# Kernel optimization log

Measured on AMD Instinct MI355X. Metric: run time of the kernel, lower is better.

## Reference

```python
import jax, jax.numpy as jnp
import numpy as np

M, K, N = 4096, 4096, 11008  # tokens, in_features, out_features


def setup_inputs() -> dict:
    key = jax.random.key(0)
    k0, k1, k2 = jax.random.split(key, 3)
    # quint8 activations: values in [0, 255], zero_point 128
    x_q = jax.random.randint(k0, (M, K), 0, 256, dtype=jnp.int32)
    # qint8 weight: values in [-128, 127], zero_point 0 (as prepacked in __init__)
    w_q = jax.random.randint(k1, (N, K), -128, 128, dtype=jnp.int32)
    bias = jax.random.normal(k2, (N,), dtype=jnp.float32) * 0.1
    return {
        "x_q": x_q,
        "w_q": w_q,
        "bias": bias,
        "x_scale": jnp.float32(0.02),
        "w_scale": jnp.float32(0.01),
        "out_scale": jnp.float32(1.0),   # self.scale = 1.0
        "x_zero_point": 128,
        "out_zero_point": 0,             # self.zero_point = 0
    }


def reference(x_q, w_q, bias, x_scale, w_scale, out_scale, x_zero_point, out_zero_point):
    # int8 GEMM with int32 accumulation: (x - zp_x) @ W^T
    acc = jnp.einsum(
        "mk,nk->mn",
        x_q - x_zero_point,
        w_q,
        preferred_element_type=jnp.int32,
    )
    # dequantize + bias (fp32), then requantize to quint8 output
    y = acc.astype(jnp.float32) * (x_scale * w_scale) + bias
    q = jnp.clip(jnp.round(y / out_scale) + out_zero_point, 0, 255).astype(jnp.int32)
    return q
```

## Files before the change

kernel.cpp:

```cpp
#include <hip/hip_runtime.h>

#define M_DIM 4096
#define K_DIM 4096
#define N_DIM 11008
#define BM 256
#define BN 128
#define BK 64
#define NTILES (K_DIM / BK)

typedef int v4i  __attribute__((ext_vector_type(4)));
typedef int v16i __attribute__((ext_vector_type(16)));

#define WAIT_VM6 0x3F76
#define WAIT_VM0 0x3F70

__device__ __forceinline__ void load_lds16(const void* g, void* l) {
    __builtin_amdgcn_global_load_lds(
        (const __attribute__((address_space(1))) void*)g,
        (__attribute__((address_space(3))) void*)l,
        16, 0, 0);
}

__device__ __forceinline__ unsigned int pack4(int4 v, int zp) {
    return ((unsigned int)(v.x - zp) & 0xFF)
         | (((unsigned int)(v.y - zp) & 0xFF) << 8)
         | (((unsigned int)(v.z - zp) & 0xFF) << 16)
         | (((unsigned int)(v.w - zp) & 0xFF) << 24);
}

__global__ void pack_both_kernel(const int* __restrict__ x, const int* __restrict__ w,
                                 unsigned int* __restrict__ x8, unsigned int* __restrict__ w8,
                                 const int* __restrict__ zp_p, int nx16, int nw16) {
    int i = blockIdx.x * blockDim.x + threadIdx.x;
    if (i < nx16) {
        const int zp = zp_p[0];
        const int4* p = (const int4*)x + i * 4;
        uint4 o;
        o.x = pack4(p[0], zp);
        o.y = pack4(p[1], zp);
        o.z = pack4(p[2], zp);
        o.w = pack4(p[3], zp);
        ((uint4*)x8)[i] = o;
    } else {
        int j = i - nx16;
        if (j >= nw16) return;
        const int4* p = (const int4*)w + j * 4;
        uint4 o;
        o.x = pack4(p[0], 0);
        o.y = pack4(p[1], 0);
        o.z = pack4(p[2], 0);
        o.w = pack4(p[3], 0);
        ((uint4*)w8)[j] = o;
    }
}

__global__ __launch_bounds__(256, 2) void gemm_i8_kernel(
    const signed char* __restrict__ A8,
    const signed char* __restrict__ B8,
    const float* __restrict__ bias,
    const float* __restrict__ xs_p, const float* __restrict__ ws_p,
    const float* __restrict__ os_p, const int* __restrict__ ozp_p,
    int* __restrict__ out) {
    __shared__ v4i As0[BM * BK / 16];
    __shared__ v4i Bs0[BN * BK / 16];
    __shared__ v4i As1[BM * BK / 16];
    __shared__ v4i Bs1[BN * BK / 16];

    const int tid  = threadIdx.x;
    const int lane = tid & 63;
    const int wave = tid >> 6;

    const int bid   = blockIdx.x;
    const int xcd   = bid & 7;
    const int local = bid >> 3;
    const int m_blk = xcd * 2 + (local >= 86 ? 1 : 0);
    const int n_blk = (local >= 86) ? (local - 86) : local;
    const int m0 = m_blk * BM;
    const int n0 = n_blk * BN;

    long offA[4], offB[2];
    int  ldsA[4], ldsB[2];
#pragma unroll
    for (int j = 0; j < 4; ++j) {
        const int s   = tid + 256 * j;
        const int row = s >> 2;
        const int gg  = (s & 3) ^ ((row >> 1) & 3);
        offA[j] = (long)(m0 + row) * K_DIM + gg * 16;
        ldsA[j] = s;
    }
#pragma unroll
    for (int j = 0; j < 2; ++j) {
        const int s   = tid + 256 * j;
        const int row = s >> 2;
        const int gg  = (s & 3) ^ ((row >> 1) & 3);
        offB[j] = (long)(n0 + row) * K_DIM + gg * 16;
        ldsB[j] = s;
    }

    const int waveM = wave >> 1, waveN = wave & 1;
    const int l31 = lane & 31, h = lane >> 5;
    int aSlot[4][2], bSlot[2][2];
#pragma unroll
    for (int mt = 0; mt < 4; ++mt) {
        const int rA = waveM * 128 + mt * 32 + l31;
#pragma unroll
        for (int s = 0; s < 2; ++s) {
            const int g = 2 * s + h;
            aSlot[mt][s] = rA * 4 + (g ^ ((rA >> 1) & 3));
        }
    }
#pragma unroll
    for (int nt = 0; nt < 2; ++nt) {
        const int rB = waveN * 64 + nt * 32 + l31;
#pragma unroll
        for (int s = 0; s < 2; ++s) {
            const int g = 2 * s + h;
            bSlot[nt][s] = rB * 4 + (g ^ ((rB >> 1) & 3));
        }
    }

    v16i acc[4][2];
#pragma unroll
    for (int mt = 0; mt < 4; ++mt)
#pragma unroll
        for (int nt = 0; nt < 2; ++nt)
#pragma unroll
            for (int r = 0; r < 16; ++r) acc[mt][nt][r] = 0;

    auto stage = [&](int tile, v4i* Asb, v4i* Bsb) {
        const long koff = (long)tile * BK;
#pragma unroll
        for (int j = 0; j < 4; ++j) load_lds16(A8 + offA[j] + koff, (char*)(Asb + ldsA[j]));
#pragma unroll
        for (int j = 0; j < 2; ++j) load_lds16(B8 + offB[j] + koff, (char*)(Bsb + ldsB[j]));
    };
    auto compute = [&](const v4i* Asb, const v4i* Bsb) {
#pragma unroll
        for (int s = 0; s < 2; ++s) {
            v4i a[4], b[2];
#pragma unroll
            for (int mt = 0; mt < 4; ++mt) a[mt] = Asb[aSlot[mt][s]];
#pragma unroll
            for (int nt = 0; nt < 2; ++nt) b[nt] = Bsb[bSlot[nt][s]];
#pragma unroll
            for (int mt = 0; mt < 4; ++mt)
#pragma unroll
                for (int nt = 0; nt < 2; ++nt)
                    acc[mt][nt] = __builtin_amdgcn_mfma_i32_32x32x32_i8(
                        a[mt], b[nt], acc[mt][nt], 0, 0, 0);
        }
    };

    stage(0, As0, Bs0);
    stage(1, As1, Bs1);

#pragma unroll 1
    for (int kk = 0; kk < 31; ++kk) {
        const int k = 2 * kk;
        __builtin_amdgcn_s_waitcnt(WAIT_VM6);
        __builtin_amdgcn_s_barrier();
        compute(As0, Bs0);
        __builtin_amdgcn_s_barrier();
        stage(k + 2, As0, Bs0);
        __builtin_amdgcn_s_waitcnt(WAIT_VM6);
        __builtin_amdgcn_s_barrier();
        compute(As1, Bs1);
        __builtin_amdgcn_s_barrier();
        stage(k + 3, As1, Bs1);
    }
    __builtin_amdgcn_s_waitcnt(WAIT_VM6);
    __builtin_amdgcn_s_barrier();
    compute(As0, Bs0);
    __builtin_amdgcn_s_waitcnt(WAIT_VM0);
    __builtin_amdgcn_s_barrier();
    compute(As1, Bs1);

    const float scale  = xs_p[0] * ws_p[0];
    const float inv_os = 1.0f / os_p[0];
    const int   ozp    = ozp_p[0];
#pragma unroll
    for (int mt = 0; mt < 4; ++mt) {
        const int rbase = m0 + waveM * 128 + mt * 32 + 4 * h;
#pragma unroll
        for (int nt = 0; nt < 2; ++nt) {
            const int col = n0 + waveN * 64 + nt * 32 + l31;
            const float bv = bias[col];
#pragma unroll
            for (int r = 0; r < 16; ++r) {
                const int row = rbase + (r & 3) + 8 * (r >> 2);
                float y = (float)acc[mt][nt][r] * scale + bv;
                int q = (int)rintf(y * inv_os) + ozp;
                q = q < 0 ? 0 : (q > 255 ? 255 : q);
                out[(long)row * N_DIM + col] = q;
            }
        }
    }
}

extern "C" void kernel_launch(void* const* d_in, const int* in_sizes, int n_in,
                              void* d_out, int out_size, void* d_ws, size_t ws_size,
                              hipStream_t stream) {
    const int*   x_q  = (const int*)d_in[0];
    const int*   w_q  = (const int*)d_in[1];
    const float* bias = (const float*)d_in[2];
    const float* xs   = (const float*)d_in[3];
    const float* wsc  = (const float*)d_in[4];
    const float* os   = (const float*)d_in[5];
    const int*   xzp  = (const int*)d_in[6];
    const int*   ozp  = (const int*)d_in[7];

    signed char* x8 = (signed char*)d_ws;
    signed char* w8 = (signed char*)d_ws + (size_t)M_DIM * K_DIM;

    const int nx16 = M_DIM * K_DIM / 16;
    const int nw16 = N_DIM * K_DIM / 16;
    const int npack = nx16 + nw16;
    pack_both_kernel<<<(npack + 255) / 256, 256, 0, stream>>>(
        x_q, w_q, (unsigned int*)x8, (unsigned int*)w8, xzp, nx16, nw16);

    const int nblocks = (M_DIM / BM) * (N_DIM / BN);
    gemm_i8_kernel<<<nblocks, 256, 0, stream>>>(x8, w8, bias, xs, wsc, os, ozp, (int*)d_out);
}
```

Before: 533.7 us.

## Shrink block tile to 128x128 and switch to 16x16x64 int8 MFMA

Halves the M block tile from 256 to 128, giving each wave a 64x64 sub-tile computed with 16x16x64 int8 MFMAs instead of 32x32x32. The block-to-XCD mapping is reworked for the doubled grid, and launch bounds are raised to target three blocks per CU. The aim is higher occupancy and better wave balance, at the cost of lower arithmetic intensity per block and more global and LDS traffic per output element.

```diff
diff --git a/kernel.cpp b/kernel.cpp
--- a/kernel.cpp
+++ b/kernel.cpp
@@ -3,15 +3,14 @@
 #define M_DIM 4096
 #define K_DIM 4096
 #define N_DIM 11008
-#define BM 256
+#define BM 128
 #define BN 128
 #define BK 64
 #define NTILES (K_DIM / BK)
 
 typedef int v4i  __attribute__((ext_vector_type(4)));
-typedef int v16i __attribute__((ext_vector_type(16)));
-
-#define WAIT_VM6 0x3F76
+
+#define WAIT_VM4 0x3F74
 #define WAIT_VM0 0x3F70
 
 __device__ __forceinline__ void load_lds16(const void* g, void* l) {
@@ -54,7 +53,7 @@
     }
 }
 
-__global__ __launch_bounds__(256, 2) void gemm_i8_kernel(
+__global__ __launch_bounds__(256, 3) void gemm_i8_kernel(
     const signed char* __restrict__ A8,
     const signed char* __restrict__ B8,
     const float* __restrict__ bias,
@@ -73,82 +72,62 @@
     const int bid   = blockIdx.x;
     const int xcd   = bid & 7;
     const int local = bid >> 3;
-    const int m_blk = xcd * 2 + (local >= 86 ? 1 : 0);
-    const int n_blk = (local >= 86) ? (local - 86) : local;
+    const int m_blk = xcd * 4 + (local & 3);
+    const int n_blk = local >> 2;
     const int m0 = m_blk * BM;
     const int n0 = n_blk * BN;
 
-    long offA[4], offB[2];
-    int  ldsA[4], ldsB[2];
-#pragma unroll
-    for (int j = 0; j < 4; ++j) {
+    long offA[2], offB[2];
+    int  ldsA[2], ldsB[2];
+#pragma unroll
+    for (int j = 0; j < 2; ++j) {
         const int s   = tid + 256 * j;
         const int row = s >> 2;
         const int gg  = (s & 3) ^ ((row >> 1) & 3);
         offA[j] = (long)(m0 + row) * K_DIM + gg * 16;
+        offB[j] = (long)(n0 + row) * K_DIM + gg * 16;
         ldsA[j] = s;
-    }
-#pragma unroll
-    for (int j = 0; j < 2; ++j) {
-        const int s   = tid + 256 * j;
-        const int row = s >> 2;
-        const int gg  = (s & 3) ^ ((row >> 1) & 3);
-        offB[j] = (long)(n0 + row) * K_DIM + gg * 16;
         ldsB[j] = s;
     }
 
     const int waveM = wave >> 1, waveN = wave & 1;
-    const int l31 = lane & 31, h = lane >> 5;
-    int aSlot[4][2], bSlot[2][2];
-#pragma unroll
-    for (int mt = 0; mt < 4; ++mt) {
-        const int rA = waveM * 128 + mt * 32 + l31;
-#pragma unroll
-        for (int s = 0; s < 2; ++s) {
-            const int g = 2 * s + h;
-            aSlot[mt][s] = rA * 4 + (g ^ ((rA >> 1) & 3));
-        }
-    }
-#pragma unroll
-    for (int nt = 0; nt < 2; ++nt) {
-        const int rB = waveN * 64 + nt * 32 + l31;
-#pragma unroll
-        for (int s = 0; s < 2; ++s) {
-            const int g = 2 * s + h;
-            bSlot[nt][s] = rB * 4 + (g ^ ((rB >> 1) & 3));
-        }
-    }
-
-    v16i acc[4][2];
-#pragma unroll
-    for (int mt = 0; mt < 4; ++mt)
-#pragma unroll
-        for (int nt = 0; nt < 2; ++nt)
-#pragma unroll
-            for (int r = 0; r < 16; ++r) acc[mt][nt][r] = 0;
+    const int l15 = lane & 15, kg = lane >> 4;
+    int aSlot[4], bSlot[4];
+#pragma unroll
+    for (int t = 0; t < 4; ++t) {
+        const int rA = waveM * 64 + t * 16 + l15;
+        const int rB = waveN * 64 + t * 16 + l15;
+        aSlot[t] = rA * 4 + (kg ^ ((rA >> 1) & 3));
+        bSlot[t] = rB * 4 + (kg ^ ((rB >> 1) & 3));
+    }
+
+    v4i acc[4][4];
+#pragma unroll
+    for (int mi = 0; mi < 4; ++mi)
+#pragma unroll
+        for (int ni = 0; ni < 4; ++ni)
+#pragma unroll
+            for (int r = 0; r < 4; ++r) acc[mi][ni][r] = 0;
 
     auto stage = [&](int tile, v4i* Asb, v4i* Bsb) {
         const long koff = (long)tile * BK;
 #pragma unroll
-        for (int j = 0; j < 4; ++j) load_lds16(A8 + offA[j] + koff, (char*)(Asb + ldsA[j]));
+        for (int j = 0; j < 2; ++j) load_lds16(A8 + offA[j] + koff, (char*)(Asb + ldsA[j]));
 #pragma unroll
         for (int j = 0; j < 2; ++j) load_lds16(B8 + offB[j] + koff, (char*)(Bsb + ldsB[j]));
     };
     auto compute = [&](const v4i* Asb, const v4i* Bsb) {
-#pragma unroll
-        for (int s = 0; s < 2; ++s) {
-            v4i a[4], b[2];
-#pragma unroll
-            for (int mt = 0; mt < 4; ++mt) a[mt] = Asb[aSlot[mt][s]];
-#pragma unroll
-            for (int nt = 0; nt < 2; ++nt) b[nt] = Bsb[bSlot[nt][s]];
-#pragma unroll
-            for (int mt = 0; mt < 4; ++mt)
-#pragma unroll
-                for (int nt = 0; nt < 2; ++nt)
-                    acc[mt][nt] = __builtin_amdgcn_mfma_i32_32x32x32_i8(
-                        a[mt], b[nt], acc[mt][nt], 0, 0, 0);
-        }
+        v4i a[4], b[4];
+#pragma unroll
+        for (int t = 0; t < 4; ++t) a[t] = Asb[aSlot[t]];
+#pragma unroll
+        for (int t = 0; t < 4; ++t) b[t] = Bsb[bSlot[t]];
+#pragma unroll
+        for (int mi = 0; mi < 4; ++mi)
+#pragma unroll
+            for (int ni = 0; ni < 4; ++ni)
+                acc[mi][ni] = __builtin_amdgcn_mfma_i32_16x16x64_i8(
+                    a[mi], b[ni], acc[mi][ni], 0, 0, 0);
     };
 
     stage(0, As0, Bs0);
@@ -157,18 +136,18 @@
 #pragma unroll 1
     for (int kk = 0; kk < 31; ++kk) {
         const int k = 2 * kk;
-        __builtin_amdgcn_s_waitcnt(WAIT_VM6);
+        __builtin_amdgcn_s_waitcnt(WAIT_VM4);
         __builtin_amdgcn_s_barrier();
         compute(As0, Bs0);
         __builtin_amdgcn_s_barrier();
         stage(k + 2, As0, Bs0);
-        __builtin_amdgcn_s_waitcnt(WAIT_VM6);
+        __builtin_amdgcn_s_waitcnt(WAIT_VM4);
         __builtin_amdgcn_s_barrier();
         compute(As1, Bs1);
         __builtin_amdgcn_s_barrier();
         stage(k + 3, As1, Bs1);
     }
-    __builtin_amdgcn_s_waitcnt(WAIT_VM6);
+    __builtin_amdgcn_s_waitcnt(WAIT_VM4);
     __builtin_amdgcn_s_barrier();
     compute(As0, Bs0);
     __builtin_amdgcn_s_waitcnt(WAIT_VM0);
@@ -179,16 +158,16 @@
     const float inv_os = 1.0f / os_p[0];
     const int   ozp    = ozp_p[0];
 #pragma unroll
-    for (int mt = 0; mt < 4; ++mt) {
-        const int rbase = m0 + waveM * 128 + mt * 32 + 4 * h;
-#pragma unroll
-        for (int nt = 0; nt < 2; ++nt) {
-            const int col = n0 + waveN * 64 + nt * 32 + l31;
+    for (int mi = 0; mi < 4; ++mi) {
+        const int rbase = m0 + waveM * 64 + mi * 16 + 4 * kg;
+#pragma unroll
+        for (int ni = 0; ni < 4; ++ni) {
+            const int col = n0 + waveN * 64 + ni * 16 + l15;
             const float bv = bias[col];
 #pragma unroll
-            for (int r = 0; r < 16; ++r) {
-                const int row = rbase + (r & 3) + 8 * (r >> 2);
-                float y = (float)acc[mt][nt][r] * scale + bv;
+            for (int r = 0; r < 4; ++r) {
+                const int row = rbase + r;
+                float y = (float)acc[mi][ni][r] * scale + bv;
                 int q = (int)rintf(y * inv_os) + ozp;
                 q = q < 0 ? 0 : (q > 255 ? 255 : q);
                 out[(long)row * N_DIM + col] = q;
```

After: 544.1 us. About the same (+1.9%).
